# Kernel optimization log

Hardware: AMD Instinct MI355X
Metric: run time of the kernel (lower is better)

## Reference

```python
import jax, jax.numpy as jnp
import numpy as np

NUM_LEVELS = 16
COARSEST = 16
FINEST = 1024
TABLE_SIZE = 524288  # max_hash_table_entries per level
FEAT = 2             # hash_table_feature_dim
DENSITY_W = 64
COLOR_W = 64
N_POINTS = 262144

PRIMES = jnp.array([1, 2654435761, 805459861], dtype=jnp.uint32)
# 8 cube corners: 1 -> ceil coordinate, 0 -> floor coordinate (matches source vertex_0..vertex_7)
CORNER_SEL = np.array([[1,1,1],[1,1,0],[1,0,1],[0,1,1],[1,0,0],[0,1,0],[0,0,1],[0,0,0]], dtype=bool)


def hash_encode(position, hash_table):
    # position: (N,3) in [0,1); hash_table: (NUM_LEVELS*TABLE_SIZE, FEAT)
    levels = jnp.arange(NUM_LEVELS)
    growth = jnp.exp((jnp.log(float(FINEST)) - jnp.log(float(COARSEST))) / (NUM_LEVELS - 1))
    scalings = jnp.floor(COARSEST * growth ** levels)            # (L,)
    scaled = position[:, None, :] * scalings[None, :, None]       # (N,L,3)
    floor = jnp.floor(scaled)
    ceil = jnp.ceil(scaled)
    sel = jnp.asarray(CORNER_SEL)[None, None]                     # (1,1,8,3)
    corners = jnp.where(sel, ceil[:, :, None, :], floor[:, :, None, :]).astype(jnp.uint32)  # (N,L,8,3)
    h = corners * PRIMES                                          # uint32 wrap-around mul
    idx = jnp.bitwise_xor(jnp.bitwise_xor(h[..., 0], h[..., 1]), h[..., 2]) % TABLE_SIZE
    idx = idx + (levels[None, :, None] * TABLE_SIZE).astype(jnp.uint32)  # (N,L,8)
    feats = hash_table[idx]                                       # (N,L,8,F) gather
    frac = scaled - floor                                         # (N,L,3)
    w = jnp.prod(jnp.where(sel, frac[:, :, None, :], 1.0 - frac[:, :, None, :]), axis=-1)  # (N,L,8)
    out = jnp.sum(feats * w[..., None], axis=2)                   # trilinear interp -> (N,L,F)
    return out.reshape(out.shape[0], NUM_LEVELS * FEAT)           # (N,32)


def sh_encode(d):
    # fourth-order spherical harmonics, vectorized over (N,3)
    x, y, z = d[:, 0], d[:, 1], d[:, 2]
    xx, yy, zz = x * x, y * y, z * z
    comps = [
        0.28209479177387814 * jnp.ones_like(x),
        0.4886025119029199 * y,
        0.4886025119029199 * z,
        0.4886025119029199 * x,
        1.0925484305920792 * x * y,
        1.0925484305920792 * y * z,
        0.9461746957575601 * zz - 0.31539156525252,
        1.0925484305920792 * x * z,
        0.5462742152960396 * (xx - yy),
        0.5900435899266435 * y * (3 * xx - yy),
        2.890611442640554 * x * y * z,
        0.4570457994644658 * y * (5 * zz - 1),
        0.3731763325901154 * z * (5 * zz - 3),
        0.4570457994644658 * x * (5 * zz - 1),
        1.445305721320277 * z * (xx - yy),
        0.5900435899266435 * x * (xx - 3 * yy),
    ]
    return jnp.stack(comps, axis=-1)  # (N,16)


def setup_inputs() -> dict:
    key = jax.random.key(0)
    ks = jax.random.split(key, 16)
    N = N_POINTS
    position = jax.random.uniform(ks[0], (N, 3), dtype=jnp.float32)
    direction = jax.random.normal(ks[1], (N, 3), dtype=jnp.float32)
    hash_table = jax.random.normal(ks[2], (NUM_LEVELS * TABLE_SIZE, FEAT), dtype=jnp.float32) * 1e-2
    enc_dim = NUM_LEVELS * FEAT  # 32
    def dense(k, fi, fo):
        return jax.random.normal(k, (fi, fo), dtype=jnp.float32) * (1.0 / np.sqrt(fi))
    return {
        "position": position,
        "direction": direction,
        "hash_table": hash_table,
        "w_d1": dense(ks[3], enc_dim, DENSITY_W), "b_d1": jnp.zeros((DENSITY_W,), jnp.float32),
        "w_d2": dense(ks[4], DENSITY_W, 16),      "b_d2": jnp.zeros((16,), jnp.float32),
        "w_c1": dense(ks[5], 16 + 16, COLOR_W),   "b_c1": jnp.zeros((COLOR_W,), jnp.float32),
        "w_c2": dense(ks[6], COLOR_W, COLOR_W),   "b_c2": jnp.zeros((COLOR_W,), jnp.float32),
        "w_c3": dense(ks[7], COLOR_W, 3),         "b_c3": jnp.zeros((3,), jnp.float32),
    }


def reference(position, direction, hash_table, w_d1, b_d1, w_d2, b_d2,
              w_c1, b_c1, w_c2, b_c2, w_c3, b_c3):
    enc_pos = hash_encode(position, hash_table)               # (N,32)
    h = jax.nn.relu(enc_pos @ w_d1 + b_d1)                    # (N,64)
    density = h @ w_d2 + b_d2                                 # (N,16)
    enc_dir = sh_encode(direction)                            # (N,16)
    x = jnp.concatenate([density, enc_dir], axis=-1)          # (N,32)
    x = jax.nn.relu(x @ w_c1 + b_c1)
    x = jax.nn.relu(x @ w_c2 + b_c2)
    x = x @ w_c3 + b_c3                                       # (N,3)
    color = jax.nn.sigmoid(x)                                 # high_dynamic_range=False
    return (density, color)
```

## Files before the change

### kernel.cpp

```cpp
#include <hip/hip_runtime.h>
#include <stdint.h>

#define NPTS 262144
#define TBL 524288u
#define TBL_MASK 524287u
#define NBINS 32768

#define WS_TAB_OFF   0u
#define WS_TAB_BYTES (8u * 524288u * 4u)
#define WS_ENC_OFF   WS_TAB_BYTES
#define WS_ENC_BYTES (16u * (uint32_t)NPTS * 4u)
#define WS_W_OFF     (WS_ENC_OFF + WS_ENC_BYTES)
#define WS_W_U32     4736
#define WS_HIST_OFF  (WS_W_OFF + WS_W_U32 * 4u)
#define WS_KEY_OFF   (WS_HIST_OFF + NBINS * 4u)
#define WS_IDX_OFF   (WS_KEY_OFF + (uint32_t)NPTS * 4u)
#define WS_PS_OFF    (WS_IDX_OFF + (uint32_t)NPTS * 4u)
#define WS_DS_OFF    (WS_PS_OFF + (uint32_t)NPTS * 12u)
#define WS_NEED_SORT ((size_t)WS_DS_OFF + (size_t)NPTS * 12u)
#define WS_NEED      ((size_t)WS_HIST_OFF)

#define PW_D1 0
#define PW_D2 1024
#define PW_C1 1536
#define PW_C2 2560
#define PW_C3 4608

typedef __attribute__((ext_vector_type(8))) _Float16 half8;
typedef __attribute__((ext_vector_type(4))) float f32x4;

__device__ const float d_scale[16] = {16.f, 21.f, 27.f, 36.f, 48.f, 64.f, 84.f, 111.f,
                                      147.f, 194.f, 256.f, 337.f, 445.f, 588.f, 776.f, 1024.f};

__device__ __forceinline__ uint16_t f2h(float f) {
    _Float16 h = (_Float16)f;
    return __builtin_bit_cast(uint16_t, h);
}
__device__ __forceinline__ uint32_t pack2(float lo, float hi) {
    return (uint32_t)f2h(lo) | ((uint32_t)f2h(hi) << 16);
}
__device__ __forceinline__ float h2f_lo(uint32_t v) {
    return (float)__builtin_bit_cast(_Float16, (uint16_t)(v & 0xffffu));
}
__device__ __forceinline__ float h2f_hi(uint32_t v) {
    return (float)__builtin_bit_cast(_Float16, (uint16_t)(v >> 16));
}

__device__ __forceinline__ half8 bfrag_p(const uint32_t* __restrict__ Wp, int N, int kofs, int nofs, int l) {
    const int kp0 = (kofs + ((l >> 4) << 3)) >> 1;
    const uint32_t* p = Wp + (size_t)kp0 * N + (nofs + (l & 15));
    union { uint32_t u[4]; half8 s; } r;
    r.u[0] = p[0 * N];
    r.u[1] = p[1 * N];
    r.u[2] = p[2 * N];
    r.u[3] = p[3 * N];
    return r.s;
}
__device__ __forceinline__ half8 bfrag3_p(const uint32_t* __restrict__ Wp, int kofs, int l) {
    const int kp0 = (kofs + ((l >> 4) << 3)) >> 1;
    const int n = l & 15;
    union { uint32_t u[4]; half8 s; } r;
    if (n < 3) {
        const uint32_t* p = Wp + (size_t)kp0 * 4 + n;
        r.u[0] = p[0]; r.u[1] = p[4]; r.u[2] = p[8]; r.u[3] = p[12];
    } else {
        r.u[0] = 0; r.u[1] = 0; r.u[2] = 0; r.u[3] = 0;
    }
    return r.s;
}

__device__ __forceinline__ half8 ld_a_h(const unsigned char* hcb, int mt, int kb, int l) {
    const int row = mt * 16 + (l & 15);
    uint32_t byte = (uint32_t)row * 128 + (uint32_t)kb * 64 + (uint32_t)((l >> 4) << 4);
    byte ^= (uint32_t)(row & 7) << 4;
    return *(const half8*)(hcb + byte);
}
__device__ __forceinline__ void st_h(unsigned char* hcb, int row, int col, float v) {
    uint32_t byte = (uint32_t)row * 128 + (uint32_t)col * 2;
    byte ^= (uint32_t)(row & 7) << 4;
    *(uint16_t*)(hcb + byte) = f2h(fmaxf(v, 0.f));
}

#define MFMA(a, b, c) __builtin_amdgcn_mfma_f32_16x16x32_f16((a), (b), (c), 0, 0, 0)

__device__ __forceinline__ uint32_t spread3(uint32_t x) {
    x &= 0x3FFu;
    x = (x | (x << 16)) & 0x030000FFu;
    x = (x | (x << 8))  & 0x0300F00Fu;
    x = (x | (x << 4))  & 0x030C30C3u;
    x = (x | (x << 2))  & 0x09249249u;
    return x;
}

__global__ void __launch_bounds__(256) khist(
    const float* __restrict__ g_pos, uint32_t* __restrict__ key, uint32_t* __restrict__ hist)
{
    const int p = blockIdx.x * 256 + threadIdx.x;
    const float px = g_pos[3 * p + 0];
    const float py = g_pos[3 * p + 1];
    const float pz = g_pos[3 * p + 2];
    const uint32_t cx = min(31u, (uint32_t)(px * 32.f));
    const uint32_t cy = min(31u, (uint32_t)(py * 32.f));
    const uint32_t cz = min(31u, (uint32_t)(pz * 32.f));
    const uint32_t k = spread3(cx) | (spread3(cy) << 1) | (spread3(cz) << 2);
    key[p] = k;
    atomicAdd(&hist[k], 1u);
}

__global__ void __launch_bounds__(1024) kscan(uint32_t* __restrict__ hist) {
    const int tid = threadIdx.x;
    const int lane = tid & 63, wid = tid >> 6;
    uint4* hp = (uint4*)(hist + tid * 32);
    uint4 a[8];
    #pragma unroll
    for (int i = 0; i < 8; ++i) a[i] = hp[i];
    uint32_t S = 0;
    #pragma unroll
    for (int i = 0; i < 8; ++i) S += a[i].x + a[i].y + a[i].z + a[i].w;

    uint32_t s = S;
    #pragma unroll
    for (int d = 1; d < 64; d <<= 1) {
        const uint32_t t = __shfl_up(s, d);
        if (lane >= d) s += t;
    }
    __shared__ uint32_t ws[16];
    if (lane == 63) ws[wid] = s;
    __syncthreads();
    uint32_t woff = 0;
    for (int w = 0; w < wid; ++w) woff += ws[w];
    uint32_t run = woff + (s - S);

    #pragma unroll
    for (int i = 0; i < 8; ++i) {
        uint4 v = a[i];
        uint4 o;
        o.x = run; run += v.x;
        o.y = run; run += v.y;
        o.z = run; run += v.z;
        o.w = run; run += v.w;
        hp[i] = o;
    }
}

__global__ void __launch_bounds__(256) convert_scatter(
    const float4* __restrict__ t8,
    uint4* __restrict__ o,
    const float* __restrict__ wd1, const float* __restrict__ wd2,
    const float* __restrict__ wc1, const float* __restrict__ wc2,
    const float* __restrict__ wc3, uint32_t* __restrict__ wp,
    const float* __restrict__ g_pos, const float* __restrict__ g_dir,
    const uint32_t* __restrict__ key,
    uint32_t* __restrict__ hist, uint32_t* __restrict__ out_idx,
    float* __restrict__ pos_sorted, float* __restrict__ dir_sorted,
    const int scatter_blocks)
{
    const int blk = blockIdx.x;
    if (blk < scatter_blocks) {
        const int p = blk * 256 + threadIdx.x;
        const uint32_t slot = atomicAdd(&hist[key[p]], 1u);
        out_idx[slot] = (uint32_t)p;
        pos_sorted[3 * slot + 0] = g_pos[3 * p + 0];
        pos_sorted[3 * slot + 1] = g_pos[3 * p + 1];
        pos_sorted[3 * slot + 2] = g_pos[3 * p + 2];
        dir_sorted[3 * slot + 0] = g_dir[3 * p + 0];
        dir_sorted[3 * slot + 1] = g_dir[3 * p + 1];
        dir_sorted[3 * slot + 2] = g_dir[3 * p + 2];
    } else {
        const int cb = blk - scatter_blocks;
        const int i = cb * 256 + threadIdx.x;
        const float4 a = t8[2 * i];
        const float4 b = t8[2 * i + 1];
        o[i] = make_uint4(pack2(a.x, a.y), pack2(a.z, a.w),
                          pack2(b.x, b.y), pack2(b.z, b.w));
        if (cb == 0) {
            const int tid = threadIdx.x;
            for (int j = tid; j < 1024; j += 256) {
                const int kp = j >> 6, n = j & 63;
                wp[PW_D1 + j] = pack2(wd1[(2 * kp) * 64 + n], wd1[(2 * kp + 1) * 64 + n]);
            }
            for (int j = tid; j < 512; j += 256) {
                const int kp = j >> 4, n = j & 15;
                wp[PW_D2 + j] = pack2(wd2[(2 * kp) * 16 + n], wd2[(2 * kp + 1) * 16 + n]);
            }
            for (int j = tid; j < 1024; j += 256) {
                const int kp = j >> 6, n = j & 63;
                wp[PW_C1 + j] = pack2(wc1[(2 * kp) * 64 + n], wc1[(2 * kp + 1) * 64 + n]);
            }
            for (int j = tid; j < 2048; j += 256) {
                const int kp = j >> 6, n = j & 63;
                wp[PW_C2 + j] = pack2(wc2[(2 * kp) * 64 + n], wc2[(2 * kp + 1) * 64 + n]);
            }
            for (int j = tid; j < 128; j += 256) {
                const int kp = j >> 2, n = j & 3;
                wp[PW_C3 + j] = (n < 3) ? pack2(wc3[(2 * kp) * 3 + n], wc3[(2 * kp + 1) * 3 + n]) : 0u;
            }
        }
    }
}

__global__ void __launch_bounds__(256) gather_enc2(
    const float* __restrict__ pos,
    const float* __restrict__ g_tab32,
    const uint32_t* __restrict__ tab16,
    uint32_t* __restrict__ enc)
{
    const int b = blockIdx.x;
    const int x8 = b & 7;
    const int lev = (b >> 12) ? (15 - x8) : x8;
    const int pbase = (((b >> 3) & 511) << 9) + threadIdx.x;

    const float s = d_scale[lev];

    float tx[2], ty[2], tz[2];
    uint32_t idx0[2][4], idx1[2][4];
    bool odd[2];
    #pragma unroll
    for (int q = 0; q < 2; ++q) {
        const int p = pbase + q * 256;
        const float px = pos[3 * p + 0];
        const float py = pos[3 * p + 1];
        const float pz = pos[3 * p + 2];
        const float sx = px * s, sy = py * s, sz = pz * s;
        const float fx = floorf(sx), fy = floorf(sy), fz = floorf(sz);
        tx[q] = sx - fx; ty[q] = sy - fy; tz[q] = sz - fz;
        const uint32_t x0 = (uint32_t)fx, x1 = (uint32_t)ceilf(sx);
        const uint32_t hy0 = (uint32_t)fy * 2654435761u, hy1 = (uint32_t)ceilf(sy) * 2654435761u;
        const uint32_t hz0 = (uint32_t)fz * 805459861u,  hz1 = (uint32_t)ceilf(sz) * 805459861u;
        odd[q] = (x0 & 1u) != 0u;
        #pragma unroll
        for (int cp = 0; cp < 4; ++cp) {
            const uint32_t hyz = ((cp & 1) ? hy1 : hy0) ^ ((cp & 2) ? hz1 : hz0);
            idx0[q][cp] = (x0 ^ hyz) & TBL_MASK;
            idx1[q][cp] = (x1 ^ hyz) & TBL_MASK;
        }
    }

    float e[2][2] = {{0.f, 0.f}, {0.f, 0.f}};
    if (lev >= 8) {
        const uint32_t* t = tab16 + (size_t)(lev - 8) * TBL;
        uint2 v2[2][4];
        #pragma unroll
        for (int q = 0; q < 2; ++q)
            #pragma unroll
            for (int cp = 0; cp < 4; ++cp)
                v2[q][cp] = *reinterpret_cast<const uint2*>(t + (idx0[q][cp] & ~1u));
        uint32_t fup[2][4];
        #pragma unroll
        for (int q = 0; q < 2; ++q)
            #pragma unroll
            for (int cp = 0; cp < 4; ++cp)
                fup[q][cp] = odd[q] ? t[idx1[q][cp]] : 0u;
        #pragma unroll
        for (int q = 0; q < 2; ++q) {
            #pragma unroll
            for (int cp = 0; cp < 4; ++cp) {
                const bool lo = (idx0[q][cp] & 1u) == 0u;
                const uint32_t v0 = lo ? v2[q][cp].x : v2[q][cp].y;
                uint32_t v1 = lo ? v2[q][cp].y : v2[q][cp].x;
                if (odd[q]) v1 = fup[q][cp];
                const float wyz = ((cp & 1) ? ty[q] : 1.f - ty[q]) * ((cp & 2) ? tz[q] : 1.f - tz[q]);
                const float w0 = (1.f - tx[q]) * wyz;
                const float w1 = tx[q] * wyz;
                e[q][0] = fmaf(h2f_lo(v0), w0, fmaf(h2f_lo(v1), w1, e[q][0]));
                e[q][1] = fmaf(h2f_hi(v0), w0, fmaf(h2f_hi(v1), w1, e[q][1]));
            }
        }
    } else {
        const float2* t = (const float2*)g_tab32 + (size_t)lev * TBL;
        float4 v2[2][4];
        #pragma unroll
        for (int q = 0; q < 2; ++q)
            #pragma unroll
            for (int cp = 0; cp < 4; ++cp)
                v2[q][cp] = *reinterpret_cast<const float4*>(t + (idx0[q][cp] & ~1u));
        float2 fup[2][4];
        #pragma unroll
        for (int q = 0; q < 2; ++q)
            #pragma unroll
            for (int cp = 0; cp < 4; ++cp)
                fup[q][cp] = odd[q] ? t[idx1[q][cp]] : make_float2(0.f, 0.f);
        #pragma unroll
        for (int q = 0; q < 2; ++q) {
            #pragma unroll
            for (int cp = 0; cp < 4; ++cp) {
                const bool lo = (idx0[q][cp] & 1u) == 0u;
                const float v0x = lo ? v2[q][cp].x : v2[q][cp].z;
                const float v0y = lo ? v2[q][cp].y : v2[q][cp].w;
                float v1x = lo ? v2[q][cp].z : v2[q][cp].x;
                float v1y = lo ? v2[q][cp].w : v2[q][cp].y;
                if (odd[q]) { v1x = fup[q][cp].x; v1y = fup[q][cp].y; }
                const float wyz = ((cp & 1) ? ty[q] : 1.f - ty[q]) * ((cp & 2) ? tz[q] : 1.f - tz[q]);
                const float w0 = (1.f - tx[q]) * wyz;
                const float w1 = tx[q] * wyz;
                e[q][0] = fmaf(v0x, w0, fmaf(v1x, w1, e[q][0]));
                e[q][1] = fmaf(v0y, w0, fmaf(v1y, w1, e[q][1]));
            }
        }
    }
    #pragma unroll
    for (int q = 0; q < 2; ++q)
        enc[(size_t)lev * NPTS + pbase + q * 256] = pack2(e[q][0], e[q][1]);
}

__global__ void __launch_bounds__(256, 3) nerf_mlp(
    const float* __restrict__ g_dir,
    const uint32_t* __restrict__ enc,
    const uint32_t* __restrict__ wp,
    const uint32_t* __restrict__ out_idx,
    const int use_perm,
    const float* __restrict__ g_bd1,
    const float* __restrict__ g_bd2,
    const float* __restrict__ g_bc1,
    const float* __restrict__ g_bc2,
    const float* __restrict__ g_bc3,
    float* __restrict__ g_out)
{
    __shared__ __align__(16) unsigned char s_lds[4 * 12288];
    unsigned char* wbase = s_lds + (threadIdx.x >> 6) * 12288;
    unsigned char* hcb  = wbase;
    unsigned char* xinb = wbase + 8192;

    const int l = threadIdx.x & 63;
    const int m_my = l >> 4;
    const int r_my = l & 15;
    const int wpt  = blockIdx.x * 256 + (threadIdx.x & 192);
    const int p    = wpt + l;

    #pragma unroll
    for (int kb = 0; kb < 4; ++kb) {
        uint4 w4;
        w4.x = enc[(size_t)(4 * kb + 0) * NPTS + p];
        w4.y = enc[(size_t)(4 * kb + 1) * NPTS + p];
        w4.z = enc[(size_t)(4 * kb + 2) * NPTS + p];
        w4.w = enc[(size_t)(4 * kb + 3) * NPTS + p];
        *(uint4*)(hcb + m_my * 1024 + (kb * 16 + r_my) * 16) = w4;
    }

    const float dx = g_dir[3 * p + 0];
    const float dy = g_dir[3 * p + 1];
    const float dz = g_dir[3 * p + 2];

    {
        const float xx = dx * dx, yy = dy * dy, zz = dz * dz;
        float s[16];
        s[0]  = 0.28209479177387814f;
        s[1]  = 0.4886025119029199f * dy;
        s[2]  = 0.4886025119029199f * dz;
        s[3]  = 0.4886025119029199f * dx;
        s[4]  = 1.0925484305920792f * dx * dy;
        s[5]  = 1.0925484305920792f * dy * dz;
        s[6]  = 0.9461746957575601f * zz - 0.31539156525252f;
        s[7]  = 1.0925484305920792f * dx * dz;
        s[8]  = 0.5462742152960396f * (xx - yy);
        s[9]  = 0.5900435899266435f * dy * (3.f * xx - yy);
        s[10] = 2.890611442640554f * dx * dy * dz;
        s[11] = 0.4570457994644658f * dy * (5.f * zz - 1.f);
        s[12] = 0.3731763325901154f * dz * (5.f * zz - 3.f);
        s[13] = 0.4570457994644658f * dx * (5.f * zz - 1.f);
        s[14] = 1.445305721320277f * dz * (xx - yy);
        s[15] = 0.5900435899266435f * dx * (xx - 3.f * yy);
        *(uint4*)(xinb + m_my * 1024 + (32 + r_my) * 16) =
            make_uint4(pack2(s[0], s[1]), pack2(s[2], s[3]), pack2(s[4], s[5]), pack2(s[6], s[7]));
        *(uint4*)(xinb + m_my * 1024 + (48 + r_my) * 16) =
            make_uint4(pack2(s[8], s[9]), pack2(s[10], s[11]), pack2(s[12], s[13]), pack2(s[14], s[15]));
    }

    const int cl = l & 15;
    const int rg = (l >> 4) << 2;

    {
        f32x4 acc[4][4];
        half8 B[4];
        #pragma unroll
        for (int nt = 0; nt < 4; ++nt) {
            B[nt] = bfrag_p(wp + PW_D1, 64, 0, nt * 16, l);
            const float b = g_bd1[nt * 16 + cl];
            #pragma unroll
            for (int mt = 0; mt < 4; ++mt) acc[mt][nt] = (f32x4){b, b, b, b};
        }
        #pragma unroll
        for (int mt = 0; mt < 4; ++mt) {
            const half8 A = *(const half8*)(hcb + mt * 1024 + l * 16);
            #pragma unroll
            for (int nt = 0; nt < 4; ++nt) acc[mt][nt] = MFMA(A, B[nt], acc[mt][nt]);
        }
        #pragma unroll
        for (int mt = 0; mt < 4; ++mt)
            #pragma unroll
            for (int nt = 0; nt < 4; ++nt)
                #pragma unroll
                for (int r = 0; r < 4; ++r)
                    st_h(hcb, mt * 16 + rg + r, nt * 16 + cl, acc[mt][nt][r]);
    }

    {
        const half8 B0 = bfrag_p(wp + PW_D2, 16, 0,  0, l);
        const half8 B1 = bfrag_p(wp + PW_D2, 16, 32, 0, l);
        const float b = g_bd2[cl];
        #pragma unroll
        for (int mt = 0; mt < 4; ++mt) {
            f32x4 acc = (f32x4){b, b, b, b};
            acc = MFMA(ld_a_h(hcb, mt, 0, l), B0, acc);
            acc = MFMA(ld_a_h(hcb, mt, 1, l), B1, acc);
            #pragma unroll
            for (int r = 0; r < 4; ++r) {
                const int pt = wpt + mt * 16 + rg + r;
                const uint32_t opt = use_perm ? out_idx[pt] : (uint32_t)pt;
                g_out[(size_t)opt * 16 + cl] = acc[r];
                const uint32_t byte = (uint32_t)mt * 1024
                                    + (uint32_t)(((cl >> 3) * 16 + rg + r) * 16) + (uint32_t)(cl & 7) * 2;
                *(uint16_t*)(xinb + byte) = f2h(acc[r]);
            }
        }
    }

    {
        f32x4 acc[4][4];
        half8 B[4];
        #pragma unroll
        for (int nt = 0; nt < 4; ++nt) {
            B[nt] = bfrag_p(wp + PW_C1, 64, 0, nt * 16, l);
            const float b = g_bc1[nt * 16 + cl];
            #pragma unroll
            for (int mt = 0; mt < 4; ++mt) acc[mt][nt] = (f32x4){b, b, b, b};
        }
        #pragma unroll
        for (int mt = 0; mt < 4; ++mt) {
            const half8 A = *(const half8*)(xinb + mt * 1024 + l * 16);
            #pragma unroll
            for (int nt = 0; nt < 4; ++nt) acc[mt][nt] = MFMA(A, B[nt], acc[mt][nt]);
        }
        #pragma unroll
        for (int mt = 0; mt < 4; ++mt)
            #pragma unroll
            for (int nt = 0; nt < 4; ++nt)
                #pragma unroll
                for (int r = 0; r < 4; ++r)
                    st_h(hcb, mt * 16 + rg + r, nt * 16 + cl, acc[mt][nt][r]);
    }

    {
        f32x4 acc[4][4];
        #pragma unroll
        for (int nt = 0; nt < 4; ++nt) {
            const float b = g_bc2[nt * 16 + cl];
            #pragma unroll
            for (int mt = 0; mt < 4; ++mt) acc[mt][nt] = (f32x4){b, b, b, b};
        }
        #pragma unroll
        for (int kb = 0; kb < 2; ++kb) {
            half8 A[4];
            #pragma unroll
            for (int mt = 0; mt < 4; ++mt) A[mt] = ld_a_h(hcb, mt, kb, l);
            #pragma unroll
            for (int nt = 0; nt < 4; ++nt) {
                const half8 B = bfrag_p(wp + PW_C2, 64, kb * 32, nt * 16, l);
                #pragma unroll
                for (int mt = 0; mt < 4; ++mt) acc[mt][nt] = MFMA(A[mt], B, acc[mt][nt]);
            }
        }
        #pragma unroll
        for (int mt = 0; mt < 4; ++mt)
            #pragma unroll
            for (int nt = 0; nt < 4; ++nt)
                #pragma unroll
                for (int r = 0; r < 4; ++r)
                    st_h(hcb, mt * 16 + rg + r, nt * 16 + cl, acc[mt][nt][r]);
    }

    {
        const half8 B0 = bfrag3_p(wp + PW_C3, 0, l);
        const half8 B1 = bfrag3_p(wp + PW_C3, 32, l);
        const float b = (cl < 3) ? g_bc3[cl] : 0.f;
        #pragma unroll
        for (int mt = 0; mt < 4; ++mt) {
            f32x4 acc = (f32x4){b, b, b, b};
            acc = MFMA(ld_a_h(hcb, mt, 0, l), B0, acc);
            acc = MFMA(ld_a_h(hcb, mt, 1, l), B1, acc);
            if (cl < 3) {
                #pragma unroll
                for (int r = 0; r < 4; ++r) {
                    const int pt = wpt + mt * 16 + rg + r;
                    const uint32_t opt = use_perm ? out_idx[pt] : (uint32_t)pt;
                    g_out[(size_t)NPTS * 16 + (size_t)opt * 3 + cl] = 1.f / (1.f + expf(-acc[r]));
                }
            }
        }
    }
}

extern "C" void kernel_launch(void* const* d_in, const int* in_sizes, int n_in,
                              void* d_out, int out_size, void* d_ws, size_t ws_size,
                              hipStream_t stream) {
    uint32_t* tab16 = (uint32_t*)((char*)d_ws + WS_TAB_OFF);
    uint32_t* enc   = (uint32_t*)((char*)d_ws + WS_ENC_OFF);
    uint32_t* wpk   = (uint32_t*)((char*)d_ws + WS_W_OFF);
    uint32_t* hist  = (uint32_t*)((char*)d_ws + WS_HIST_OFF);
    uint32_t* key   = (uint32_t*)((char*)d_ws + WS_KEY_OFF);
    uint32_t* oidx  = (uint32_t*)((char*)d_ws + WS_IDX_OFF);
    float*    psort = (float*)((char*)d_ws + WS_PS_OFF);
    float*    dsort = (float*)((char*)d_ws + WS_DS_OFF);

    const float* g_pos = (const float*)d_in[0];
    const float* g_dir = (const float*)d_in[1];
    const float* g_tab = (const float*)d_in[2];
    const float4* t8 = (const float4*)(g_tab + (size_t)2 * 8 * TBL);

    if (ws_size >= WS_NEED_SORT) {
        hipMemsetAsync(hist, 0, NBINS * 4, stream);
        khist<<<NPTS / 256, 256, 0, stream>>>(g_pos, key, hist);
        kscan<<<1, 1024, 0, stream>>>(hist);
        convert_scatter<<<1024 + 4096, 256, 0, stream>>>(
            t8, (uint4*)tab16,
            (const float*)d_in[3], (const float*)d_in[5],
            (const float*)d_in[7], (const float*)d_in[9],
            (const float*)d_in[11], wpk,
            g_pos, g_dir, key, hist, oidx, psort, dsort, 1024);
        gather_enc2<<<8192, 256, 0, stream>>>(psort, g_tab, tab16, enc);
        nerf_mlp<<<NPTS / 256, 256, 0, stream>>>(
            dsort, enc, wpk, oidx, 1,
            (const float*)d_in[4], (const float*)d_in[6],
            (const float*)d_in[8], (const float*)d_in[10],
            (const float*)d_in[12],
            (float*)d_out);
    } else {
        convert_scatter<<<4096, 256, 0, stream>>>(
            t8, (uint4*)tab16,
            (const float*)d_in[3], (const float*)d_in[5],
            (const float*)d_in[7], (const float*)d_in[9],
            (const float*)d_in[11], wpk,
            g_pos, g_dir, nullptr, nullptr, nullptr, nullptr, nullptr, 0);
        gather_enc2<<<8192, 256, 0, stream>>>(g_pos, g_tab, tab16, enc);
        nerf_mlp<<<NPTS / 256, 256, 0, stream>>>(
            g_dir, enc, wpk, nullptr, 0,
            (const float*)d_in[4], (const float*)d_in[6],
            (const float*)d_in[8], (const float*)d_in[10],
            (const float*)d_in[12],
            (float*)d_out);
    }
}
```

Baseline: 158.3 us.

## Convert levels 5-15 to fp16 table and rebalance level-to-block schedule

Extends the fp16 copy of the hash table from levels 8-15 to levels 5-15, so more levels gather packed half features instead of fp32. A per-XCD segment table replaces the simple level interleave and assigns point chunks of different levels to each x8 lane to balance gather cost. The conversion kernel launches more blocks to convert the extra three levels. This adds conversion traffic and workspace in exchange for lower gather bandwidth on mid levels, with slightly reduced precision there.

```diff
diff --git a/kernel.cpp b/kernel.cpp
--- a/kernel.cpp
+++ b/kernel.cpp
@@ -7,7 +7,7 @@
 #define NBINS 32768
 
 #define WS_TAB_OFF   0u
-#define WS_TAB_BYTES (8u * 524288u * 4u)
+#define WS_TAB_BYTES (11u * 524288u * 4u)
 #define WS_ENC_OFF   WS_TAB_BYTES
 #define WS_ENC_BYTES (16u * (uint32_t)NPTS * 4u)
 #define WS_W_OFF     (WS_ENC_OFF + WS_ENC_BYTES)
@@ -31,6 +31,25 @@
 
 __device__ const float d_scale[16] = {16.f, 21.f, 27.f, 36.f, 48.f, 64.f, 84.f, 111.f,
                                       147.f, 194.f, 256.f, 337.f, 445.f, 588.f, 776.f, 1024.f};
+
+__device__ const uint16_t SEG_START[8][4] = {
+    {0, 512, 683, 1024},
+    {0, 512, 683, 854},
+    {0, 512, 682, 1024},
+    {0, 512, 768, 1024},
+    {0, 512, 768, 1024},
+    {0, 512, 768, 1024},
+    {0, 512, 768, 1024},
+    {0, 512, 1024, 1024},
+};
+__device__ const int8_t SEG_LEV[8][4] = {
+    {9, 7, 2, 0}, {10, 7, 2, 1}, {11, 7, 1, 0}, {12, 6, 0, 0},
+    {13, 6, 0, 0}, {14, 4, 3, 0}, {15, 4, 3, 0}, {8, 5, 0, 0},
+};
+__device__ const uint16_t SEG_CB[8][4] = {
+    {0, 0, 0, 0}, {0, 171, 341, 0}, {0, 342, 170, 0}, {0, 0, 0, 0},
+    {0, 256, 256, 0}, {0, 0, 0, 0}, {0, 256, 256, 0}, {0, 0, 0, 0},
+};
 
 __device__ __forceinline__ uint16_t f2h(float f) {
     _Float16 h = (_Float16)f;
@@ -144,7 +163,7 @@
 }
 
 __global__ void __launch_bounds__(256) convert_scatter(
-    const float4* __restrict__ t8,
+    const float4* __restrict__ t5,
     uint4* __restrict__ o,
     const float* __restrict__ wd1, const float* __restrict__ wd2,
     const float* __restrict__ wc1, const float* __restrict__ wc2,
@@ -169,8 +188,8 @@
     } else {
         const int cb = blk - scatter_blocks;
         const int i = cb * 256 + threadIdx.x;
-        const float4 a = t8[2 * i];
-        const float4 b = t8[2 * i + 1];
+        const float4 a = t5[2 * i];
+        const float4 b = t5[2 * i + 1];
         o[i] = make_uint4(pack2(a.x, a.y), pack2(a.z, a.w),
                           pack2(b.x, b.y), pack2(b.z, b.w));
         if (cb == 0) {
@@ -207,8 +226,13 @@
 {
     const int b = blockIdx.x;
     const int x8 = b & 7;
-    const int lev = (b >> 12) ? (15 - x8) : x8;
-    const int pbase = (((b >> 3) & 511) << 9) + threadIdx.x;
+    const int sslot = b >> 3;
+    int seg = 0;
+    #pragma unroll
+    for (int i = 1; i < 4; ++i) seg = (sslot >= (int)SEG_START[x8][i]) ? i : seg;
+    const int lev = SEG_LEV[x8][seg];
+    const int chunk = (int)SEG_CB[x8][seg] + (sslot - (int)SEG_START[x8][seg]);
+    const int pbase = (chunk << 9) + threadIdx.x;
 
     const float s = d_scale[lev];
 
@@ -237,8 +261,8 @@
     }
 
     float e[2][2] = {{0.f, 0.f}, {0.f, 0.f}};
-    if (lev >= 8) {
-        const uint32_t* t = tab16 + (size_t)(lev - 8) * TBL;
+    if (lev >= 5) {
+        const uint32_t* t = tab16 + (size_t)(lev - 5) * TBL;
         uint2 v2[2][4];
         #pragma unroll
         for (int q = 0; q < 2; ++q)
@@ -505,14 +529,14 @@
     const float* g_pos = (const float*)d_in[0];
     const float* g_dir = (const float*)d_in[1];
     const float* g_tab = (const float*)d_in[2];
-    const float4* t8 = (const float4*)(g_tab + (size_t)2 * 8 * TBL);
+    const float4* t5 = (const float4*)(g_tab + (size_t)2 * 5 * TBL);
 
     if (ws_size >= WS_NEED_SORT) {
         hipMemsetAsync(hist, 0, NBINS * 4, stream);
         khist<<<NPTS / 256, 256, 0, stream>>>(g_pos, key, hist);
         kscan<<<1, 1024, 0, stream>>>(hist);
-        convert_scatter<<<1024 + 4096, 256, 0, stream>>>(
-            t8, (uint4*)tab16,
+        convert_scatter<<<1024 + 5632, 256, 0, stream>>>(
+            t5, (uint4*)tab16,
             (const float*)d_in[3], (const float*)d_in[5],
             (const float*)d_in[7], (const float*)d_in[9],
             (const float*)d_in[11], wpk,
@@ -525,8 +549,8 @@
             (const float*)d_in[12],
             (float*)d_out);
     } else {
-        convert_scatter<<<4096, 256, 0, stream>>>(
-            t8, (uint4*)tab16,
+        convert_scatter<<<5632, 256, 0, stream>>>(
+            t5, (uint4*)tab16,
             (const float*)d_in[3], (const float*)d_in[5],
             (const float*)d_in[7], (const float*)d_in[9],
             (const float*)d_in[11], wpk,
```

Result: slower. 164.2 us (+3.7%).
